# Optimization experiments

Hardware: AMD Instinct MI355X
Metric: run time of the kernel (lower is better)

Reference implementation:

```python
import jax, jax.numpy as jnp
import numpy as np

B, N, T = 64, 65536, 8      # batch, tag locations (256x256 heatmap), tag_dim
M, K = 30, 17               # max people, joints per person (COCO)


def setup_inputs() -> dict:
    key = jax.random.key(0)
    k1, k2, k3 = jax.random.split(key, 3)
    tags = jax.random.normal(k1, (B, N, T), dtype=jnp.float32)
    idx = jax.random.randint(k2, (B, M, K), 0, N)          # pixel index per joint
    valid = jax.random.randint(k3, (B, M, K), 0, 2)        # validity flag {0,1}
    keypoints = jnp.stack([idx, valid], axis=-1)           # [B, M, K, 2] int
    return {"tags": tags, "keypoints": keypoints}


def _ae_loss(tags, keypoints):
    # tags: [B, N, T] float; keypoints: [B, M, K, 2] int (index, valid)
    Bn, Nn, Tn = tags.shape
    Mn, Kn = keypoints.shape[1], keypoints.shape[2]
    idx = keypoints[..., 0]                                   # [B, M, K]
    vf = (keypoints[..., 1] > 0).astype(tags.dtype)           # [B, M, K]

    # gather tag vectors at keypoint locations -> [B, M, K, T]
    g = jnp.take_along_axis(tags, idx.reshape(Bn, Mn * Kn, 1), axis=1)
    g = g.reshape(Bn, Mn, Kn, Tn)

    cnt = vf.sum(axis=2)                                      # [B, M] valid joints/person
    has = cnt > 0                                             # [B, M] person present
    safe_cnt = jnp.maximum(cnt, 1.0)
    mean = (g * vf[..., None]).sum(axis=2) / safe_cnt[..., None]   # [B, M, T]

    # pull: per person, mean over valid joints (and tag dim) of squared diff to mean
    sq = ((g - mean[:, :, None, :]) ** 2).mean(axis=-1)       # [B, M, K]
    pull_p = (sq * vf).sum(axis=2) / safe_cnt                 # [B, M]
    n = has.astype(tags.dtype).sum(axis=1)                    # [B] num people
    pull = pull_p.sum(axis=1) / jnp.maximum(n, 1.0)           # [B]

    # push: exp(-||mean_i - mean_j||^2) over distinct valid person pairs
    d2 = ((mean[:, :, None, :] - mean[:, None, :, :]) ** 2).sum(-1)   # [B, M, M]
    pair = has[:, :, None] & has[:, None, :]
    pair = pair & ~jnp.eye(Mn, dtype=bool)[None]
    push = jnp.where(pair, jnp.exp(-d2), 0.0).sum(axis=(1, 2))        # [B]
    denom = jnp.maximum(n * (n - 1.0), 1.0)
    push = jnp.where(n > 1, push / denom * 0.5, 0.0)

    return jnp.stack([push, pull], axis=-1)                   # [B, 2]


def reference(tags, keypoints):
    return _ae_loss(tags, keypoints)
```

## Files before the change

### kernel.cpp

```cpp
#include <hip/hip_runtime.h>


#define Bc 64
#define Nc 65536
#define Tc 8
#define Mc 30
#define Kc 17

__global__ __launch_bounds__(256) void ae_loss_kernel(
    const float* __restrict__ tags,
    const int*   __restrict__ kp,
    float*       __restrict__ out)
{
    const int b   = blockIdx.x;
    const int tid = threadIdx.x;

    __shared__ float g[Mc * Kc * Tc];
    __shared__ float vf[Mc * Kc];
    __shared__ float mean_s[Mc * Tc];
    __shared__ float pull_p[Mc];
    __shared__ float cnt_s[Mc];
    __shared__ float wsum[4];

    const float* tb = tags + (size_t)b * Nc * Tc;
    const int*   kb = kp   + (size_t)b * Mc * Kc * 2;

    for (int p = tid; p < Mc * Kc; p += 256) {
        int idx = kb[2 * p];
        int v   = kb[2 * p + 1];
        vf[p] = (v > 0) ? 1.0f : 0.0f;
        const float4* src = (const float4*)(tb + (size_t)idx * Tc);
        float4 a = src[0];
        float4 c = src[1];
        float* gd = g + p * Tc;
        *(float4*)(gd)     = a;
        *(float4*)(gd + 4) = c;
    }
    __syncthreads();

    if (tid < Mc) {
        const int m = tid;
        float c = 0.0f;
        float s[Tc];
        #pragma unroll
        for (int t = 0; t < Tc; ++t) s[t] = 0.0f;

        for (int k = 0; k < Kc; ++k) {
            float v = vf[m * Kc + k];
            c += v;
            #pragma unroll
            for (int t = 0; t < Tc; ++t)
                s[t] += g[(m * Kc + k) * Tc + t] * v;
        }
        float sc  = fmaxf(c, 1.0f);
        float inv = 1.0f / sc;
        #pragma unroll
        for (int t = 0; t < Tc; ++t) {
            s[t] *= inv;
            mean_s[m * Tc + t] = s[t];
        }
        float pp = 0.0f;
        for (int k = 0; k < Kc; ++k) {
            float sq = 0.0f;
            #pragma unroll
            for (int t = 0; t < Tc; ++t) {
                float d = g[(m * Kc + k) * Tc + t] - s[t];
                sq += d * d;
            }
            pp += (sq * 0.125f) * vf[m * Kc + k];
        }
        pull_p[m] = pp * inv;
        cnt_s[m]  = c;
    }
    __syncthreads();

    float local = 0.0f;
    for (int p = tid; p < Mc * Mc; p += 256) {
        int i = p / Mc;
        int j = p - i * Mc;
        if (i != j && cnt_s[i] > 0.0f && cnt_s[j] > 0.0f) {
            float d2 = 0.0f;
            #pragma unroll
            for (int t = 0; t < Tc; ++t) {
                float d = mean_s[i * Tc + t] - mean_s[j * Tc + t];
                d2 += d * d;
            }
            local += expf(-d2);
        }
    }
    #pragma unroll
    for (int off = 32; off > 0; off >>= 1)
        local += __shfl_down(local, off, 64);
    if ((tid & 63) == 0) wsum[tid >> 6] = local;
    __syncthreads();

    if (tid == 0) {
        float push_tot = wsum[0] + wsum[1] + wsum[2] + wsum[3];
        float n = 0.0f, pull = 0.0f;
        for (int m = 0; m < Mc; ++m) {
            n    += (cnt_s[m] > 0.0f) ? 1.0f : 0.0f;
            pull += pull_p[m];
        }
        pull /= fmaxf(n, 1.0f);
        float push = 0.0f;
        if (n > 1.0f)
            push = push_tot / fmaxf(n * (n - 1.0f), 1.0f) * 0.5f;
        out[2 * b + 0] = push;
        out[2 * b + 1] = pull;
    }
}

extern "C" void kernel_launch(void* const* d_in, const int* in_sizes, int n_in,
                              void* d_out, int out_size, void* d_ws, size_t ws_size,
                              hipStream_t stream) {
    const float* tags = (const float*)d_in[0];
    const int*   kp   = (const int*)d_in[1];
    float*       out  = (float*)d_out;
    ae_loss_kernel<<<Bc, 256, 0, stream>>>(tags, kp, out);
}
```

Measured before the change: 163.8 us.

## Parallelize per-person mean and pull computation across threads with 512-thread blocks

Raises the block size to 512 so each of the 510 keypoints is gathered by one thread in a single pass. The per-person mean is now computed by 240 threads (one per person and tag dimension), and the squared deviations by one thread per keypoint. The old single 30-thread serial loop is replaced by three parallel phases with extra barriers and a shared buffer. Only 64 blocks run, so the kernel is latency bound, and shortening the serial chain is what this targets.

```diff
diff --git a/kernel.cpp b/kernel.cpp
--- a/kernel.cpp
+++ b/kernel.cpp
@@ -6,8 +6,9 @@
 #define Tc 8
 #define Mc 30
 #define Kc 17
+#define THREADS 512
 
-__global__ __launch_bounds__(256) void ae_loss_kernel(
+__global__ __launch_bounds__(THREADS) void ae_loss_kernel(
     const float* __restrict__ tags,
     const int*   __restrict__ kp,
     float*       __restrict__ out)
@@ -18,64 +19,64 @@
     __shared__ float g[Mc * Kc * Tc];
     __shared__ float vf[Mc * Kc];
     __shared__ float mean_s[Mc * Tc];
+    __shared__ float sq_s[Mc * Kc];
+    __shared__ float cnt_s[Mc];
     __shared__ float pull_p[Mc];
-    __shared__ float cnt_s[Mc];
-    __shared__ float wsum[4];
+    __shared__ float wsum[8];
 
     const float* tb = tags + (size_t)b * Nc * Tc;
     const int*   kb = kp   + (size_t)b * Mc * Kc * 2;
 
-    for (int p = tid; p < Mc * Kc; p += 256) {
-        int idx = kb[2 * p];
-        int v   = kb[2 * p + 1];
-        vf[p] = (v > 0) ? 1.0f : 0.0f;
+    if (tid < Mc * Kc) {
+        int idx = kb[2 * tid];
+        int v   = kb[2 * tid + 1];
+        vf[tid] = (v > 0) ? 1.0f : 0.0f;
         const float4* src = (const float4*)(tb + (size_t)idx * Tc);
         float4 a = src[0];
         float4 c = src[1];
-        float* gd = g + p * Tc;
-        *(float4*)(gd)     = a;
-        *(float4*)(gd + 4) = c;
+        float* gd = g + tid * Tc;
+        ((float4*)gd)[0] = a;
+        ((float4*)gd)[1] = c;
+    }
+    __syncthreads();
+
+    if (tid < Mc * Tc) {
+        int m = tid >> 3;
+        int t = tid & 7;
+        float c = 0.0f, s = 0.0f;
+        #pragma unroll
+        for (int k = 0; k < Kc; ++k) {
+            float v = vf[m * Kc + k];
+            c += v;
+            s += g[(m * Kc + k) * Tc + t] * v;
+        }
+        float inv = 1.0f / fmaxf(c, 1.0f);
+        mean_s[tid] = s * inv;
+        if (t == 0) cnt_s[m] = c;
+    }
+    __syncthreads();
+
+    if (tid < Mc * Kc) {
+        int m = tid / Kc;
+        float sq = 0.0f;
+        #pragma unroll
+        for (int t = 0; t < Tc; ++t) {
+            float d = g[tid * Tc + t] - mean_s[m * Tc + t];
+            sq += d * d;
+        }
+        sq_s[tid] = sq * 0.125f * vf[tid];
     }
     __syncthreads();
 
     if (tid < Mc) {
-        const int m = tid;
-        float c = 0.0f;
-        float s[Tc];
+        float s = 0.0f;
         #pragma unroll
-        for (int t = 0; t < Tc; ++t) s[t] = 0.0f;
-
-        for (int k = 0; k < Kc; ++k) {
-            float v = vf[m * Kc + k];
-            c += v;
-            #pragma unroll
-            for (int t = 0; t < Tc; ++t)
-                s[t] += g[(m * Kc + k) * Tc + t] * v;
-        }
-        float sc  = fmaxf(c, 1.0f);
-        float inv = 1.0f / sc;
-        #pragma unroll
-        for (int t = 0; t < Tc; ++t) {
-            s[t] *= inv;
-            mean_s[m * Tc + t] = s[t];
-        }
-        float pp = 0.0f;
-        for (int k = 0; k < Kc; ++k) {
-            float sq = 0.0f;
-            #pragma unroll
-            for (int t = 0; t < Tc; ++t) {
-                float d = g[(m * Kc + k) * Tc + t] - s[t];
-                sq += d * d;
-            }
-            pp += (sq * 0.125f) * vf[m * Kc + k];
-        }
-        pull_p[m] = pp * inv;
-        cnt_s[m]  = c;
+        for (int k = 0; k < Kc; ++k) s += sq_s[tid * Kc + k];
+        pull_p[tid] = s / fmaxf(cnt_s[tid], 1.0f);
     }
-    __syncthreads();
 
     float local = 0.0f;
-    for (int p = tid; p < Mc * Mc; p += 256) {
+    for (int p = tid; p < Mc * Mc; p += THREADS) {
         int i = p / Mc;
         int j = p - i * Mc;
         if (i != j && cnt_s[i] > 0.0f && cnt_s[j] > 0.0f) {
@@ -95,7 +96,9 @@
     __syncthreads();
 
     if (tid == 0) {
-        float push_tot = wsum[0] + wsum[1] + wsum[2] + wsum[3];
+        float push_tot = 0.0f;
+        #pragma unroll
+        for (int w = 0; w < 8; ++w) push_tot += wsum[w];
         float n = 0.0f, pull = 0.0f;
         for (int m = 0; m < Mc; ++m) {
             n    += (cnt_s[m] > 0.0f) ? 1.0f : 0.0f;
@@ -116,5 +119,5 @@
     const float* tags = (const float*)d_in[0];
     const int*   kp   = (const int*)d_in[1];
     float*       out  = (float*)d_out;
-    ae_loss_kernel<<<Bc, 256, 0, stream>>>(tags, kp, out);
+    ae_loss_kernel<<<Bc, THREADS, 0, stream>>>(tags, kp, out);
 }
```

New measurement: 162.0 us. No clear change (-1.1%).
